# Performance work log

Measured on AMD Instinct MI355X. Metric: run time of the kernel, lower is better.

The kernel has to match this reference:

```python
import jax, jax.numpy as jnp
import numpy as np

EPS = 1e-4


def setup_inputs() -> dict:
    key = jax.random.key(0)
    ks = jax.random.split(key, 16)
    N, D, H, K = 262144, 162, 256, 30
    s = 0.05  # weight init scale
    return {
        "Yh": jax.random.uniform(ks[0], (N, D), dtype=jnp.float32),
        "u": jax.random.uniform(ks[1], (1,), dtype=jnp.float32),
        "W1": jax.random.normal(ks[2], (D, H), dtype=jnp.float32) * s,
        "b1": jnp.zeros((H,), jnp.float32),
        "W2": jax.random.normal(ks[3], (H, H), dtype=jnp.float32) * s,
        "b2": jnp.zeros((H,), jnp.float32),
        "Wa": jax.random.normal(ks[4], (H, K), dtype=jnp.float32) * s,
        "ba": jnp.zeros((K,), jnp.float32),
        "Wb": jax.random.normal(ks[5], (H, K), dtype=jnp.float32) * s,
        "bb": jnp.zeros((K,), jnp.float32),
        "Wd1": jax.random.normal(ks[6], (K, H), dtype=jnp.float32) * s,
        "bd1": jnp.zeros((H,), jnp.float32),
        "Wd2": jax.random.normal(ks[7], (H, D), dtype=jnp.float32) * s,
        "bd2": jnp.zeros((D,), jnp.float32),
    }


def _stick_segments(v):
    # pi_k = v_k * prod_{j<k} (1 - v_j)  (vectorized exclusive cumprod,
    # replacing the original per-dim Python loop)
    cp = jnp.cumprod(1.0 - v, axis=1)  # [N, K]
    excl = jnp.concatenate([jnp.ones_like(v[:, :1]), cp[:, :-1]], axis=1)
    return v * excl


def reference(Yh, u, W1, b1, W2, b2, Wa, ba, Wb, bb, Wd1, bd1, Wd2, bd2):
    # encode_hsi: dense MLP -> positive Kumaraswamy params (softplus heads)
    h = jax.nn.relu(Yh @ W1 + b1)
    h = jax.nn.relu(h @ W2 + b2)
    alpha = jax.nn.softplus(h @ Wa + ba) + EPS  # param1_hsi [N, K]
    beta = jax.nn.softplus(h @ Wb + bb) + EPS   # param2_hsi [N, K]
    # Kumaraswamy reparametrization with a single shared uniform sample
    uu = u[0] * 0.98 + 0.01  # Uniform(0.01, 0.99) scalar
    v = (1.0 - uu ** (1.0 / beta)) ** (1.0 / alpha)  # [N, K]
    # set_v_K_to_one: force last stick proportion to 1
    v = jnp.concatenate([v[:, :-1], jnp.ones_like(v[:, :1])], axis=1)
    pi_h = _stick_segments(v)  # [N, K], rows sum to 1
    # decode: MLP -> sigmoid (positive outputs, recon.log() finite)
    d = jax.nn.relu(pi_h @ Wd1 + bd1)
    recon = jax.nn.sigmoid(d @ Wd2 + bd2)  # [N, D]
    return recon, alpha, beta, pi_h
```

## Files before the change

### kernel.cpp

```cpp
#include <hip/hip_runtime.h>
#include <hip/hip_bf16.h>

#define N_ROWS 262144
#define D_IN 162
#define K_DIM 30
#define ROWS 32
#define NTHR 512

using bf16_t = __hip_bfloat16;
typedef __attribute__((ext_vector_type(8))) short bf16x8;
typedef __attribute__((ext_vector_type(4))) float f32x4;

__device__ __forceinline__ int swz_byte(int row, int col) {
  int b = (row << 9) + (col << 1);
  return b ^ ((row & 7) << 4);
}

__device__ __forceinline__ uint32_t bf16b(float x) {
  return (uint32_t)__builtin_bit_cast(unsigned short, __float2bfloat16(x));
}
__device__ __forceinline__ uint32_t pack2(float lo, float hi) {
  return bf16b(lo) | (bf16b(hi) << 16);
}
__device__ __forceinline__ float unpk_lo(uint32_t p) {
  return __bfloat162float(__builtin_bit_cast(__hip_bfloat16, (unsigned short)(p & 0xffff)));
}
__device__ __forceinline__ float unpk_hi(uint32_t p) {
  return __bfloat162float(__builtin_bit_cast(__hip_bfloat16, (unsigned short)(p >> 16)));
}

__device__ __forceinline__ float fexp2(float x) { return __builtin_amdgcn_exp2f(x); }
__device__ __forceinline__ float flog2(float x) { return __builtin_amdgcn_logf(x); }
__device__ __forceinline__ float frcp (float x) { return __builtin_amdgcn_rcpf(x); }

__device__ __forceinline__ float sp_fast(float x) {
  float e = fexp2(fabsf(x) * -1.44269504f);
  return fmaxf(x, 0.f) + 0.69314718f * flog2(1.f + e);
}
__device__ __forceinline__ float sigmoid_fast(float x) {
  return frcp(1.f + fexp2(x * -1.44269504f));
}

__global__ void pack_b_kernel(const float* __restrict__ src, bf16_t* __restrict__ dst,
                              int K, int N, int Np, int KB) {
  int idx = blockIdx.x * 256 + threadIdx.x;
  int total = KB * Np * 32;
  if (idx >= total) return;
  int ks = idx & 31;
  int n  = (idx >> 5) % Np;
  int kb = idx / (32 * Np);
  int k  = kb * 32 + ks;
  float v = (k < K && n < N) ? src[k * N + n] : 0.f;
  dst[idx] = __float2bfloat16(v);
}

__global__ void pack_ab_kernel(const float* __restrict__ Wa, const float* __restrict__ Wb,
                               bf16_t* __restrict__ dst) {
  int idx = blockIdx.x * 256 + threadIdx.x;
  if (idx >= 8 * 64 * 32) return;
  int ks = idx & 31;
  int n  = (idx >> 5) & 63;
  int kb = idx >> 11;
  int k  = kb * 32 + ks;
  int j = n >> 1, s = n & 1;
  float v = (j < K_DIM) ? (s ? Wb[k * K_DIM + j] : Wa[k * K_DIM + j]) : 0.f;
  dst[idx] = __float2bfloat16(v);
}

template<int NP, int NMO>
__device__ __forceinline__ void wload(const bf16_t* __restrict__ Wp, int kb, int ocBase,
                                      int lr, int lg, bf16x8 (&out)[NMO]) {
#pragma unroll
  for (int mo = 0; mo < NMO; ++mo)
    out[mo] = *reinterpret_cast<const bf16x8*>(
        Wp + ((kb * NP + ocBase + 16 * mo + lr) << 5) + 8 * lg);
}

template<int KB, int NP, int NMO, int NR>
__device__ __forceinline__ void gemm_direct(const uint8_t* lds, int srcOff,
                                            const bf16_t* __restrict__ Wp, int ocBase,
                                            int lr, int lg, f32x4 (&acc)[NMO][NR]) {
  int bE[NR], bO[NR];
#pragma unroll
  for (int nr = 0; nr < NR; ++nr) {
    bE[nr] = srcOff + swz_byte(16 * nr + lr, 8 * lg);
    bO[nr] = srcOff + swz_byte(16 * nr + lr, 32 + 8 * lg);
  }
#pragma unroll
  for (int kb = 0; kb < KB; ++kb) {
    bf16x8 wf[NMO];
    wload<NP, NMO>(Wp, kb, ocBase, lr, lg, wf);
    bf16x8 hf[NR];
#pragma unroll
    for (int nr = 0; nr < NR; ++nr) {
      int base = (kb & 1) ? bO[nr] : bE[nr];
      hf[nr] = *reinterpret_cast<const bf16x8*>(lds + base + (kb >> 1) * 128);
    }
#pragma unroll
    for (int mo = 0; mo < NMO; ++mo)
#pragma unroll
      for (int nr = 0; nr < NR; ++nr)
        acc[mo][nr] = __builtin_amdgcn_mfma_f32_16x16x32_bf16(wf[mo], hf[nr], acc[mo][nr], 0, 0, 0);
  }
}

template<int NMO, int NR>
__device__ __forceinline__ void acc_bias_init(const float* __restrict__ bias, int ocBase,
                                              int lg, f32x4 (&acc)[NMO][NR]) {
#pragma unroll
  for (int mo = 0; mo < NMO; ++mo) {
    float4 bv = *reinterpret_cast<const float4*>(bias + ocBase + 16 * mo + 4 * lg);
    f32x4 t = {bv.x, bv.y, bv.z, bv.w};
#pragma unroll
    for (int nr = 0; nr < NR; ++nr) acc[mo][nr] = t;
  }
}

template<int NMO, int NR>
__device__ __forceinline__ void epi_relu_store(uint8_t* lds, int dstOff, int ocBase,
                                               int lr, int lg, f32x4 (&acc)[NMO][NR]) {
#pragma unroll
  for (int mo = 0; mo < NMO; ++mo)
#pragma unroll
    for (int nr = 0; nr < NR; ++nr) {
      int row = 16 * nr + lr;
      int col = ocBase + 16 * mo + 4 * lg;
      float x0 = fmaxf(acc[mo][nr][0], 0.f), x1 = fmaxf(acc[mo][nr][1], 0.f);
      float x2 = fmaxf(acc[mo][nr][2], 0.f), x3 = fmaxf(acc[mo][nr][3], 0.f);
      uint2 p; p.x = pack2(x0, x1); p.y = pack2(x2, x3);
      *reinterpret_cast<uint2*>(lds + dstOff + swz_byte(row, col)) = p;
    }
}

template<int LG>
__device__ __forceinline__ bf16x8 scan_frag(const float* __restrict__ vrow,
                                            uint8_t* __restrict__ piPair) {
  float ex = 1.f, hold = 0.f;
  uint32_t pk0 = 0, pk1 = 0, pk2 = 0, pk3 = 0;
#pragma unroll
  for (int j = 0; j < 32; ++j) {
    float pi;
    if (j < K_DIM - 1)       { float vj = vrow[j]; pi = vj * ex; ex *= (1.f - vj); }
    else if (j == K_DIM - 1)   pi = ex;
    else                       pi = 0.f;
    if (j & 1) {
      uint32_t p = pack2(hold, pi);
      if (piPair != nullptr && j < K_DIM)
        *reinterpret_cast<uint32_t*>(piPair + (j - 1) * 2) = p;
      if (j >= 8 * LG && j < 8 * LG + 8) {
        switch ((j - 8 * LG) >> 1) {
          case 0: pk0 = p; break; case 1: pk1 = p; break;
          case 2: pk2 = p; break; default: pk3 = p;
        }
      }
    } else hold = pi;
  }
  uint4 t = make_uint4(pk0, pk1, pk2, pk3);
  return __builtin_bit_cast(bf16x8, t);
}

#define OFF_B  16384
#define OFF_PI 32768

__launch_bounds__(NTHR, 8)
__global__ void usdn_fused(const float* __restrict__ Yh, const float* __restrict__ u,
                           const float* __restrict__ b1, const float* __restrict__ b2,
                           const float* __restrict__ ba, const float* __restrict__ bb,
                           const float* __restrict__ bd1, const float* __restrict__ bd2,
                           const bf16_t* __restrict__ Wp1, const bf16_t* __restrict__ Wp2,
                           const bf16_t* __restrict__ Wpab, const bf16_t* __restrict__ Wpd1,
                           const bf16_t* __restrict__ Wpd2,
                           float* __restrict__ outRecon, float* __restrict__ outAlpha,
                           float* __restrict__ outBeta, float* __restrict__ outPi) {
  __shared__ __align__(16) uint8_t lds[35328];

  const int tid = threadIdx.x;
  const int w  = tid >> 6;
  const int l  = tid & 63;
  const int lr = l & 15;
  const int lg = l >> 4;
  const int r0 = blockIdx.x * ROWS;

  {
    const int srow = tid >> 4, s16 = tid & 15;
    const float2* src = reinterpret_cast<const float2*>(Yh + (size_t)(r0 + srow) * D_IN);
#pragma unroll
    for (int h = 0; h < 2; ++h) {
      float2 sv[3];
#pragma unroll
      for (int it = 0; it < 3; ++it) {
        int f2 = s16 + (h * 3 + it) * 16;
        if (f2 < 81) sv[it] = src[f2];
      }
#pragma unroll
      for (int it = 0; it < 3; ++it) {
        int f2 = s16 + (h * 3 + it) * 16;
        uint32_t p = 0;
        if (f2 < 81) p = pack2(sv[it].x, sv[it].y);
        *reinterpret_cast<uint32_t*>(lds + swz_byte(srow, f2 * 2)) = p;
      }
    }
  }
  __syncthreads();

  {
    f32x4 acc[2][2];
    acc_bias_init<2, 2>(b1, w * 32, lg, acc);
    gemm_direct<6, 256, 2, 2>(lds, 0, Wp1, w * 32, lr, lg, acc);
    epi_relu_store<2, 2>(lds, OFF_B, w * 32, lr, lg, acc);
  }
  __syncthreads();

  {
    f32x4 acc[2][2];
    acc_bias_init<2, 2>(b2, w * 32, lg, acc);
    gemm_direct<8, 256, 2, 2>(lds, OFF_B, Wp2, w * 32, lr, lg, acc);
    epi_relu_store<2, 2>(lds, 0, w * 32, lr, lg, acc);
  }
  __syncthreads();

  float regA[2][2], regB[2][2];
  const int j0 = 8 * w + 2 * lg;
  if (w < 4) {
    bool jv = (j0 < K_DIM);
    float ba0 = jv ? ba[j0] : 0.f,     bb0 = jv ? bb[j0] : 0.f;
    float ba1 = jv ? ba[j0 + 1] : 0.f, bb1 = jv ? bb[j0 + 1] : 0.f;
    f32x4 acc[1][2];
    f32x4 binit = {ba0, bb0, ba1, bb1};
    acc[0][0] = binit; acc[0][1] = binit;
    gemm_direct<8, 64, 1, 2>(lds, 0, Wpab, 16 * w, lr, lg, acc);

    float uu  = u[0] * 0.98f + 0.01f;
    float l2u = flog2(uu);
    float* vbuf = reinterpret_cast<float*>(lds + OFF_B);
#pragma unroll
    for (int nr = 0; nr < 2; ++nr) {
      int row = 16 * nr + lr;
      float a0  = sp_fast(acc[0][nr][0]) + 1e-4f;
      float b0v = sp_fast(acc[0][nr][1]) + 1e-4f;
      float a1  = sp_fast(acc[0][nr][2]) + 1e-4f;
      float b1v = sp_fast(acc[0][nr][3]) + 1e-4f;
      regA[nr][0] = a0; regB[nr][0] = b0v;
      regA[nr][1] = a1; regB[nr][1] = b1v;
      if (jv) {
        if (j0 < K_DIM - 1) {
          float t = fexp2(l2u * frcp(b0v));
          vbuf[row * 33 + j0] = fexp2(flog2(1.f - t) * frcp(a0));
        }
        if (j0 + 1 < K_DIM - 1) {
          float t = fexp2(l2u * frcp(b1v));
          vbuf[row * 33 + j0 + 1] = fexp2(flog2(1.f - t) * frcp(a1));
        }
      }
    }
  }
  __syncthreads();

  {
    bf16x8 pf[2];
    const float* vb = reinterpret_cast<const float*>(lds + OFF_B);
#pragma unroll
    for (int nr = 0; nr < 2; ++nr) {
      int row = 16 * nr + lr;
      const float* vrow = vb + row * 33;
      uint8_t* po = (w == 0) ? (lds + OFF_PI + row * 80) : nullptr;
      if      (lg == 0) pf[nr] = scan_frag<0>(vrow, po);
      else if (lg == 1) pf[nr] = scan_frag<1>(vrow, nullptr);
      else if (lg == 2) pf[nr] = scan_frag<2>(vrow, nullptr);
      else              pf[nr] = scan_frag<3>(vrow, nullptr);
    }
    f32x4 acc[2][2];
    acc_bias_init<2, 2>(bd1, w * 32, lg, acc);
    bf16x8 w4[2];
    wload<256, 2>(Wpd1, 0, w * 32, lr, lg, w4);
#pragma unroll
    for (int mo = 0; mo < 2; ++mo)
#pragma unroll
      for (int nr = 0; nr < 2; ++nr)
        acc[mo][nr] = __builtin_amdgcn_mfma_f32_16x16x32_bf16(w4[mo], pf[nr], acc[mo][nr], 0, 0, 0);
    epi_relu_store<2, 2>(lds, 0, w * 32, lr, lg, acc);
  }
  __syncthreads();

  if (w < 6) {
    f32x4 acc[2][2];
#pragma unroll
    for (int mo = 0; mo < 2; ++mo) {
      int col0 = 32 * w + 16 * mo + 4 * lg;
      f32x4 t;
#pragma unroll
      for (int i = 0; i < 4; ++i) t[i] = (col0 + i < D_IN) ? bd2[col0 + i] : 0.f;
#pragma unroll
      for (int nr = 0; nr < 2; ++nr) acc[mo][nr] = t;
    }
    gemm_direct<8, 192, 2, 2>(lds, 0, Wpd2, 32 * w, lr, lg, acc);
#pragma unroll
    for (int mo = 0; mo < 2; ++mo) {
      int col0 = 32 * w + 16 * mo + 4 * lg;
#pragma unroll
      for (int nr = 0; nr < 2; ++nr) {
        int row = 16 * nr + lr;
        float s0 = sigmoid_fast(acc[mo][nr][0]);
        float s1 = sigmoid_fast(acc[mo][nr][1]);
        float s2 = sigmoid_fast(acc[mo][nr][2]);
        float s3 = sigmoid_fast(acc[mo][nr][3]);
        float* dst = outRecon + (size_t)(r0 + row) * D_IN + col0;
        if (col0 < D_IN)     *reinterpret_cast<float2*>(dst)     = make_float2(s0, s1);
        if (col0 + 2 < D_IN) *reinterpret_cast<float2*>(dst + 2) = make_float2(s2, s3);
      }
    }
  }

  if (w < 4 && j0 < K_DIM) {
#pragma unroll
    for (int nr = 0; nr < 2; ++nr) {
      int row = 16 * nr + lr;
      size_t base = (size_t)(r0 + row) * K_DIM + j0;
      *reinterpret_cast<float2*>(outAlpha + base) = make_float2(regA[nr][0], regA[nr][1]);
      *reinterpret_cast<float2*>(outBeta  + base) = make_float2(regB[nr][0], regB[nr][1]);
    }
  }
  if (tid < 128) {
    int row = tid >> 2, l4 = tid & 3;
#pragma unroll
    for (int it = 0; it < 4; ++it) {
      int f2 = l4 + it * 4;
      if (f2 < 15) {
        uint32_t pp = *reinterpret_cast<const uint32_t*>(lds + OFF_PI + row * 80 + f2 * 4);
        *reinterpret_cast<float2*>(outPi + (size_t)(r0 + row) * K_DIM + f2 * 2) =
            make_float2(unpk_lo(pp), unpk_hi(pp));
      }
    }
  }
}

extern "C" void kernel_launch(void* const* d_in, const int* in_sizes, int n_in,
                              void* d_out, int out_size, void* d_ws, size_t ws_size,
                              hipStream_t stream) {
  const float* Yh  = (const float*)d_in[0];
  const float* u   = (const float*)d_in[1];
  const float* W1  = (const float*)d_in[2];
  const float* b1  = (const float*)d_in[3];
  const float* W2  = (const float*)d_in[4];
  const float* b2  = (const float*)d_in[5];
  const float* Wa  = (const float*)d_in[6];
  const float* ba  = (const float*)d_in[7];
  const float* Wb  = (const float*)d_in[8];
  const float* bb  = (const float*)d_in[9];
  const float* Wd1 = (const float*)d_in[10];
  const float* bd1 = (const float*)d_in[11];
  const float* Wd2 = (const float*)d_in[12];
  const float* bd2 = (const float*)d_in[13];

  bf16_t* ws   = (bf16_t*)d_ws;
  bf16_t* Wp1  = ws;
  bf16_t* Wp2  = Wp1 + 49152;
  bf16_t* Wpab = Wp2 + 65536;
  bf16_t* Wpd1 = Wpab + 16384;
  bf16_t* Wpd2 = Wpd1 + 8192;

  float* outRecon = (float*)d_out;
  float* outAlpha = outRecon + (size_t)N_ROWS * D_IN;
  float* outBeta  = outAlpha + (size_t)N_ROWS * K_DIM;
  float* outPi    = outBeta  + (size_t)N_ROWS * K_DIM;

  pack_b_kernel<<<192, 256, 0, stream>>>(W1, Wp1, 162, 256, 256, 6);
  pack_b_kernel<<<256, 256, 0, stream>>>(W2, Wp2, 256, 256, 256, 8);
  pack_ab_kernel<<<64, 256, 0, stream>>>(Wa, Wb, Wpab);
  pack_b_kernel<<<32, 256, 0, stream>>>(Wd1, Wpd1, 30, 256, 256, 1);
  pack_b_kernel<<<192, 256, 0, stream>>>(Wd2, Wpd2, 256, 162, 192, 8);

  usdn_fused<<<N_ROWS / ROWS, NTHR, 0, stream>>>(Yh, u, b1, b2, ba, bb, bd1, bd2,
                                                 Wp1, Wp2, Wpab, Wpd1, Wpd2,
                                                 outRecon, outAlpha, outBeta, outPi);
}
```

Before: 278.8 us.

## Process two row tiles per block in a software-pipelined, staggered stage schedule

```diff
diff --git a/kernel.cpp b/kernel.cpp
--- a/kernel.cpp
+++ b/kernel.cpp
@@ -159,10 +159,167 @@
   return __builtin_bit_cast(bf16x8, t);
 }
 
-#define OFF_B  16384
-#define OFF_PI 32768
-
-__launch_bounds__(NTHR, 8)
+__device__ __forceinline__ void p0_read(const float* __restrict__ Yh, int r0, int tid,
+                                        float2 (&sv)[6]) {
+  int srow = tid >> 4, s16 = tid & 15;
+  const float2* src = reinterpret_cast<const float2*>(Yh + (size_t)(r0 + srow) * D_IN);
+#pragma unroll
+  for (int it = 0; it < 6; ++it) {
+    int f2 = s16 + it * 16;
+    if (f2 < 81) sv[it] = src[f2];
+  }
+}
+__device__ __forceinline__ void p0_write(uint8_t* __restrict__ buf, int tid,
+                                         const float2 (&sv)[6]) {
+  int srow = tid >> 4, s16 = tid & 15;
+#pragma unroll
+  for (int it = 0; it < 6; ++it) {
+    int f2 = s16 + it * 16;
+    uint32_t p = (f2 < 81) ? pack2(sv[it].x, sv[it].y) : 0u;
+    *reinterpret_cast<uint32_t*>(buf + swz_byte(srow, f2 * 2)) = p;
+  }
+}
+
+__device__ __forceinline__ void heads_read(const uint8_t* __restrict__ buf,
+                                           const bf16_t* __restrict__ Wpab,
+                                           const float* __restrict__ ba,
+                                           const float* __restrict__ bb,
+                                           const float* __restrict__ u,
+                                           int w, int lr, int lg,
+                                           float (&vv)[2][2], float (&rA)[2][2],
+                                           float (&rB)[2][2]) {
+  if (w >= 4) return;
+  int j0 = 8 * w + 2 * lg;
+  bool jv = (j0 < K_DIM);
+  float ba0 = jv ? ba[j0] : 0.f,     bb0 = jv ? bb[j0] : 0.f;
+  float ba1 = jv ? ba[j0 + 1] : 0.f, bb1 = jv ? bb[j0 + 1] : 0.f;
+  f32x4 acc[1][2];
+  f32x4 binit = {ba0, bb0, ba1, bb1};
+  acc[0][0] = binit; acc[0][1] = binit;
+  gemm_direct<8, 64, 1, 2>(buf, 0, Wpab, 16 * w, lr, lg, acc);
+  float uu  = u[0] * 0.98f + 0.01f;
+  float l2u = flog2(uu);
+#pragma unroll
+  for (int nr = 0; nr < 2; ++nr) {
+    float a0  = sp_fast(acc[0][nr][0]) + 1e-4f;
+    float b0v = sp_fast(acc[0][nr][1]) + 1e-4f;
+    float a1  = sp_fast(acc[0][nr][2]) + 1e-4f;
+    float b1v = sp_fast(acc[0][nr][3]) + 1e-4f;
+    rA[nr][0] = a0; rB[nr][0] = b0v;
+    rA[nr][1] = a1; rB[nr][1] = b1v;
+    float t0 = fexp2(l2u * frcp(b0v));
+    vv[nr][0] = fexp2(flog2(1.f - t0) * frcp(a0));
+    float t1 = fexp2(l2u * frcp(b1v));
+    vv[nr][1] = fexp2(flog2(1.f - t1) * frcp(a1));
+  }
+}
+__device__ __forceinline__ void heads_write(uint8_t* __restrict__ buf, int w, int lr,
+                                            int lg, const float (&vv)[2][2]) {
+  if (w >= 4) return;
+  int j0 = 8 * w + 2 * lg;
+  if (j0 >= K_DIM) return;
+  float* vbuf = reinterpret_cast<float*>(buf);
+#pragma unroll
+  for (int nr = 0; nr < 2; ++nr) {
+    int row = 16 * nr + lr;
+    if (j0 < K_DIM - 1)     vbuf[row * 33 + j0]     = vv[nr][0];
+    if (j0 + 1 < K_DIM - 1) vbuf[row * 33 + j0 + 1] = vv[nr][1];
+  }
+}
+
+__device__ __forceinline__ void g4_read(uint8_t* __restrict__ buf,
+                                        uint8_t* __restrict__ piT,
+                                        const bf16_t* __restrict__ Wpd1,
+                                        const float* __restrict__ bd1,
+                                        int w, int lr, int lg, f32x4 (&acc)[2][2]) {
+  bf16x8 pf[2];
+  const float* vb = reinterpret_cast<const float*>(buf);
+#pragma unroll
+  for (int nr = 0; nr < 2; ++nr) {
+    int row = 16 * nr + lr;
+    const float* vrow = vb + row * 33;
+    uint8_t* po = (w == 0) ? (piT + row * 80) : nullptr;
+    if      (lg == 0) pf[nr] = scan_frag<0>(vrow, po);
+    else if (lg == 1) pf[nr] = scan_frag<1>(vrow, nullptr);
+    else if (lg == 2) pf[nr] = scan_frag<2>(vrow, nullptr);
+    else              pf[nr] = scan_frag<3>(vrow, nullptr);
+  }
+  acc_bias_init<2, 2>(bd1, w * 32, lg, acc);
+  bf16x8 w4[2];
+  wload<256, 2>(Wpd1, 0, w * 32, lr, lg, w4);
+#pragma unroll
+  for (int mo = 0; mo < 2; ++mo)
+#pragma unroll
+    for (int nr = 0; nr < 2; ++nr)
+      acc[mo][nr] = __builtin_amdgcn_mfma_f32_16x16x32_bf16(w4[mo], pf[nr], acc[mo][nr], 0, 0, 0);
+}
+
+__device__ __forceinline__ void g5_read(const uint8_t* __restrict__ buf,
+                                        const bf16_t* __restrict__ Wpd2,
+                                        const float* __restrict__ bd2,
+                                        int w, int lr, int lg, f32x4 (&acc)[2][2]) {
+  if (w >= 6) return;
+#pragma unroll
+  for (int mo = 0; mo < 2; ++mo) {
+    int col0 = 32 * w + 16 * mo + 4 * lg;
+    f32x4 t;
+#pragma unroll
+    for (int i = 0; i < 4; ++i) t[i] = (col0 + i < D_IN) ? bd2[col0 + i] : 0.f;
+#pragma unroll
+    for (int nr = 0; nr < 2; ++nr) acc[mo][nr] = t;
+  }
+  gemm_direct<8, 192, 2, 2>(buf, 0, Wpd2, 32 * w, lr, lg, acc);
+}
+__device__ __forceinline__ void g5_write(float* __restrict__ outRecon, int r0,
+                                         int w, int lr, int lg, f32x4 (&acc)[2][2]) {
+  if (w >= 6) return;
+#pragma unroll
+  for (int mo = 0; mo < 2; ++mo) {
+    int col0 = 32 * w + 16 * mo + 4 * lg;
+#pragma unroll
+    for (int nr = 0; nr < 2; ++nr) {
+      int row = 16 * nr + lr;
+      float s0 = sigmoid_fast(acc[mo][nr][0]);
+      float s1 = sigmoid_fast(acc[mo][nr][1]);
+      float s2 = sigmoid_fast(acc[mo][nr][2]);
+      float s3 = sigmoid_fast(acc[mo][nr][3]);
+      float* dst = outRecon + (size_t)(r0 + row) * D_IN + col0;
+      if (col0 < D_IN)     *reinterpret_cast<float2*>(dst)     = make_float2(s0, s1);
+      if (col0 + 2 < D_IN) *reinterpret_cast<float2*>(dst + 2) = make_float2(s2, s3);
+    }
+  }
+}
+__device__ __forceinline__ void ab_store(float* __restrict__ outAlpha,
+                                         float* __restrict__ outBeta, int r0,
+                                         int w, int lr, int lg,
+                                         const float (&rA)[2][2], const float (&rB)[2][2]) {
+  if (w >= 4) return;
+  int j0 = 8 * w + 2 * lg;
+  if (j0 >= K_DIM) return;
+#pragma unroll
+  for (int nr = 0; nr < 2; ++nr) {
+    int row = 16 * nr + lr;
+    size_t base = (size_t)(r0 + row) * K_DIM + j0;
+    *reinterpret_cast<float2*>(outAlpha + base) = make_float2(rA[nr][0], rA[nr][1]);
+    *reinterpret_cast<float2*>(outBeta  + base) = make_float2(rB[nr][0], rB[nr][1]);
+  }
+}
+__device__ __forceinline__ void pi_store(float* __restrict__ outPi,
+                                         const uint8_t* __restrict__ piT, int r0, int tid) {
+  if (tid >= 128) return;
+  int row = tid >> 2, l4 = tid & 3;
+#pragma unroll
+  for (int it = 0; it < 4; ++it) {
+    int f2 = l4 + it * 4;
+    if (f2 < 15) {
+      uint32_t pp = *reinterpret_cast<const uint32_t*>(piT + row * 80 + f2 * 4);
+      *reinterpret_cast<float2*>(outPi + (size_t)(r0 + row) * K_DIM + f2 * 2) =
+          make_float2(unpk_lo(pp), unpk_hi(pp));
+    }
+  }
+}
+
+__launch_bounds__(NTHR, 4)
 __global__ void usdn_fused(const float* __restrict__ Yh, const float* __restrict__ u,
                            const float* __restrict__ b1, const float* __restrict__ b2,
                            const float* __restrict__ ba, const float* __restrict__ bb,
@@ -172,165 +329,97 @@
                            const bf16_t* __restrict__ Wpd2,
                            float* __restrict__ outRecon, float* __restrict__ outAlpha,
                            float* __restrict__ outBeta, float* __restrict__ outPi) {
-  __shared__ __align__(16) uint8_t lds[35328];
+  __shared__ __align__(16) uint8_t lds[37888];
+  uint8_t* bufA = lds;
+  uint8_t* bufB = lds + 16384;
+  uint8_t* piTA = lds + 32768;
+  uint8_t* piTB = lds + 35328;
 
   const int tid = threadIdx.x;
   const int w  = tid >> 6;
   const int l  = tid & 63;
   const int lr = l & 15;
   const int lg = l >> 4;
-  const int r0 = blockIdx.x * ROWS;
-
-  {
-    const int srow = tid >> 4, s16 = tid & 15;
-    const float2* src = reinterpret_cast<const float2*>(Yh + (size_t)(r0 + srow) * D_IN);
-#pragma unroll
-    for (int h = 0; h < 2; ++h) {
-      float2 sv[3];
-#pragma unroll
-      for (int it = 0; it < 3; ++it) {
-        int f2 = s16 + (h * 3 + it) * 16;
-        if (f2 < 81) sv[it] = src[f2];
-      }
-#pragma unroll
-      for (int it = 0; it < 3; ++it) {
-        int f2 = s16 + (h * 3 + it) * 16;
-        uint32_t p = 0;
-        if (f2 < 81) p = pack2(sv[it].x, sv[it].y);
-        *reinterpret_cast<uint32_t*>(lds + swz_byte(srow, f2 * 2)) = p;
-      }
-    }
-  }
-  __syncthreads();
-
-  {
+  const int r0A = blockIdx.x * (2 * ROWS);
+  const int r0B = r0A + ROWS;
+
+  float rAA[2][2], rBA[2][2];
+  float rAB[2][2], rBB[2][2];
+
+  {
+    float2 svA[6];
+    p0_read(Yh, r0A, tid, svA);
+    p0_write(bufA, tid, svA);
+  }
+  __syncthreads();
+
+  {
+    float2 svB[6];
+    p0_read(Yh, r0B, tid, svB);
     f32x4 acc[2][2];
     acc_bias_init<2, 2>(b1, w * 32, lg, acc);
-    gemm_direct<6, 256, 2, 2>(lds, 0, Wp1, w * 32, lr, lg, acc);
-    epi_relu_store<2, 2>(lds, OFF_B, w * 32, lr, lg, acc);
-  }
-  __syncthreads();
-
-  {
-    f32x4 acc[2][2];
-    acc_bias_init<2, 2>(b2, w * 32, lg, acc);
-    gemm_direct<8, 256, 2, 2>(lds, OFF_B, Wp2, w * 32, lr, lg, acc);
-    epi_relu_store<2, 2>(lds, 0, w * 32, lr, lg, acc);
-  }
-  __syncthreads();
-
-  float regA[2][2], regB[2][2];
-  const int j0 = 8 * w + 2 * lg;
-  if (w < 4) {
-    bool jv = (j0 < K_DIM);
-    float ba0 = jv ? ba[j0] : 0.f,     bb0 = jv ? bb[j0] : 0.f;
-    float ba1 = jv ? ba[j0 + 1] : 0.f, bb1 = jv ? bb[j0 + 1] : 0.f;
-    f32x4 acc[1][2];
-    f32x4 binit = {ba0, bb0, ba1, bb1};
-    acc[0][0] = binit; acc[0][1] = binit;
-    gemm_direct<8, 64, 1, 2>(lds, 0, Wpab, 16 * w, lr, lg, acc);
-
-    float uu  = u[0] * 0.98f + 0.01f;
-    float l2u = flog2(uu);
-    float* vbuf = reinterpret_cast<float*>(lds + OFF_B);
-#pragma unroll
-    for (int nr = 0; nr < 2; ++nr) {
-      int row = 16 * nr + lr;
-      float a0  = sp_fast(acc[0][nr][0]) + 1e-4f;
-      float b0v = sp_fast(acc[0][nr][1]) + 1e-4f;
-      float a1  = sp_fast(acc[0][nr][2]) + 1e-4f;
-      float b1v = sp_fast(acc[0][nr][3]) + 1e-4f;
-      regA[nr][0] = a0; regB[nr][0] = b0v;
-      regA[nr][1] = a1; regB[nr][1] = b1v;
-      if (jv) {
-        if (j0 < K_DIM - 1) {
-          float t = fexp2(l2u * frcp(b0v));
-          vbuf[row * 33 + j0] = fexp2(flog2(1.f - t) * frcp(a0));
-        }
-        if (j0 + 1 < K_DIM - 1) {
-          float t = fexp2(l2u * frcp(b1v));
-          vbuf[row * 33 + j0 + 1] = fexp2(flog2(1.f - t) * frcp(a1));
-        }
-      }
-    }
-  }
-  __syncthreads();
-
-  {
-    bf16x8 pf[2];
-    const float* vb = reinterpret_cast<const float*>(lds + OFF_B);
-#pragma unroll
-    for (int nr = 0; nr < 2; ++nr) {
-      int row = 16 * nr + lr;
-      const float* vrow = vb + row * 33;
-      uint8_t* po = (w == 0) ? (lds + OFF_PI + row * 80) : nullptr;
-      if      (lg == 0) pf[nr] = scan_frag<0>(vrow, po);
-      else if (lg == 1) pf[nr] = scan_frag<1>(vrow, nullptr);
-      else if (lg == 2) pf[nr] = scan_frag<2>(vrow, nullptr);
-      else              pf[nr] = scan_frag<3>(vrow, nullptr);
-    }
-    f32x4 acc[2][2];
-    acc_bias_init<2, 2>(bd1, w * 32, lg, acc);
-    bf16x8 w4[2];
-    wload<256, 2>(Wpd1, 0, w * 32, lr, lg, w4);
-#pragma unroll
-    for (int mo = 0; mo < 2; ++mo)
-#pragma unroll
-      for (int nr = 0; nr < 2; ++nr)
-        acc[mo][nr] = __builtin_amdgcn_mfma_f32_16x16x32_bf16(w4[mo], pf[nr], acc[mo][nr], 0, 0, 0);
-    epi_relu_store<2, 2>(lds, 0, w * 32, lr, lg, acc);
-  }
-  __syncthreads();
-
-  if (w < 6) {
-    f32x4 acc[2][2];
-#pragma unroll
-    for (int mo = 0; mo < 2; ++mo) {
-      int col0 = 32 * w + 16 * mo + 4 * lg;
-      f32x4 t;
-#pragma unroll
-      for (int i = 0; i < 4; ++i) t[i] = (col0 + i < D_IN) ? bd2[col0 + i] : 0.f;
-#pragma unroll
-      for (int nr = 0; nr < 2; ++nr) acc[mo][nr] = t;
-    }
-    gemm_direct<8, 192, 2, 2>(lds, 0, Wpd2, 32 * w, lr, lg, acc);
-#pragma unroll
-    for (int mo = 0; mo < 2; ++mo) {
-      int col0 = 32 * w + 16 * mo + 4 * lg;
-#pragma unroll
-      for (int nr = 0; nr < 2; ++nr) {
-        int row = 16 * nr + lr;
-        float s0 = sigmoid_fast(acc[mo][nr][0]);
-        float s1 = sigmoid_fast(acc[mo][nr][1]);
-        float s2 = sigmoid_fast(acc[mo][nr][2]);
-        float s3 = sigmoid_fast(acc[mo][nr][3]);
-        float* dst = outRecon + (size_t)(r0 + row) * D_IN + col0;
-        if (col0 < D_IN)     *reinterpret_cast<float2*>(dst)     = make_float2(s0, s1);
-        if (col0 + 2 < D_IN) *reinterpret_cast<float2*>(dst + 2) = make_float2(s2, s3);
-      }
-    }
-  }
-
-  if (w < 4 && j0 < K_DIM) {
-#pragma unroll
-    for (int nr = 0; nr < 2; ++nr) {
-      int row = 16 * nr + lr;
-      size_t base = (size_t)(r0 + row) * K_DIM + j0;
-      *reinterpret_cast<float2*>(outAlpha + base) = make_float2(regA[nr][0], regA[nr][1]);
-      *reinterpret_cast<float2*>(outBeta  + base) = make_float2(regB[nr][0], regB[nr][1]);
-    }
-  }
-  if (tid < 128) {
-    int row = tid >> 2, l4 = tid & 3;
-#pragma unroll
-    for (int it = 0; it < 4; ++it) {
-      int f2 = l4 + it * 4;
-      if (f2 < 15) {
-        uint32_t pp = *reinterpret_cast<const uint32_t*>(lds + OFF_PI + row * 80 + f2 * 4);
-        *reinterpret_cast<float2*>(outPi + (size_t)(r0 + row) * K_DIM + f2 * 2) =
-            make_float2(unpk_lo(pp), unpk_hi(pp));
-      }
-    }
+    gemm_direct<6, 256, 2, 2>(bufA, 0, Wp1, w * 32, lr, lg, acc);
+    __syncthreads();
+    p0_write(bufB, tid, svB);
+    epi_relu_store<2, 2>(bufA, 0, w * 32, lr, lg, acc);
+  }
+  __syncthreads();
+
+  {
+    f32x4 accA[2][2];
+    acc_bias_init<2, 2>(b2, w * 32, lg, accA);
+    gemm_direct<8, 256, 2, 2>(bufA, 0, Wp2, w * 32, lr, lg, accA);
+    f32x4 accB[2][2];
+    acc_bias_init<2, 2>(b1, w * 32, lg, accB);
+    gemm_direct<6, 256, 2, 2>(bufB, 0, Wp1, w * 32, lr, lg, accB);
+    __syncthreads();
+    epi_relu_store<2, 2>(bufA, 0, w * 32, lr, lg, accA);
+    epi_relu_store<2, 2>(bufB, 0, w * 32, lr, lg, accB);
+  }
+  __syncthreads();
+
+  {
+    float vvA[2][2];
+    heads_read(bufA, Wpab, ba, bb, u, w, lr, lg, vvA, rAA, rBA);
+    f32x4 accB[2][2];
+    acc_bias_init<2, 2>(b2, w * 32, lg, accB);
+    gemm_direct<8, 256, 2, 2>(bufB, 0, Wp2, w * 32, lr, lg, accB);
+    __syncthreads();
+    heads_write(bufA, w, lr, lg, vvA);
+    epi_relu_store<2, 2>(bufB, 0, w * 32, lr, lg, accB);
+  }
+  __syncthreads();
+
+  {
+    f32x4 accA[2][2];
+    g4_read(bufA, piTA, Wpd1, bd1, w, lr, lg, accA);
+    float vvB[2][2];
+    heads_read(bufB, Wpab, ba, bb, u, w, lr, lg, vvB, rAB, rBB);
+    __syncthreads();
+    epi_relu_store<2, 2>(bufA, 0, w * 32, lr, lg, accA);
+    heads_write(bufB, w, lr, lg, vvB);
+  }
+  __syncthreads();
+
+  {
+    f32x4 accA[2][2];
+    g5_read(bufA, Wpd2, bd2, w, lr, lg, accA);
+    f32x4 accB[2][2];
+    g4_read(bufB, piTB, Wpd1, bd1, w, lr, lg, accB);
+    __syncthreads();
+    g5_write(outRecon, r0A, w, lr, lg, accA);
+    ab_store(outAlpha, outBeta, r0A, w, lr, lg, rAA, rBA);
+    pi_store(outPi, piTA, r0A, tid);
+    epi_relu_store<2, 2>(bufB, 0, w * 32, lr, lg, accB);
+  }
+  __syncthreads();
+
+  {
+    f32x4 accB[2][2];
+    g5_read(bufB, Wpd2, bd2, w, lr, lg, accB);
+    g5_write(outRecon, r0B, w, lr, lg, accB);
+    ab_store(outAlpha, outBeta, r0B, w, lr, lg, rAB, rBB);
+    pi_store(outPi, piTB, r0B, tid);
   }
 }
 
@@ -370,7 +459,7 @@
   pack_b_kernel<<<32, 256, 0, stream>>>(Wd1, Wpd1, 30, 256, 256, 1);
   pack_b_kernel<<<192, 256, 0, stream>>>(Wd2, Wpd2, 256, 162, 192, 8);
 
-  usdn_fused<<<N_ROWS / ROWS, NTHR, 0, stream>>>(Yh, u, b1, b2, ba, bb, bd1, bd2,
-                                                 Wp1, Wp2, Wpab, Wpd1, Wpd2,
-                                                 outRecon, outAlpha, outBeta, outPi);
-}
+  usdn_fused<<<N_ROWS / (2 * ROWS), NTHR, 0, stream>>>(Yh, u, b1, b2, ba, bb, bd1, bd2,
+                                                       Wp1, Wp2, Wpab, Wpd1, Wpd2,
+                                                       outRecon, outAlpha, outBeta, outPi);
+}
```

Measured after the change: 314.8 us. +12.9%, slower.
